# Kernel tuning notes

Hardware: AMD Instinct MI355X
Metric: run time of the kernel (lower is better)

Reference implementation:

```python
import jax, jax.numpy as jnp
import numpy as np
import math

DIM = 384
HEADS = 6
HEAD_DIM = DIM // HEADS
MLP_HIDDEN = int(DIM * 2.0)


def layer_norm(x, g, b, eps=1e-5):
    mu = jnp.mean(x, axis=-1, keepdims=True)
    var = jnp.mean((x - mu) ** 2, axis=-1, keepdims=True)
    return (x - mu) * jax.lax.rsqrt(var + eps) * g + b


def setup_inputs() -> dict:
    key = jax.random.key(0)
    ks = jax.random.split(key, 12)
    B, N = 4, 2048
    s = 0.02
    return {
        "x": jax.random.normal(ks[0], (B, N, DIM), dtype=jnp.float32),
        "pos": jax.random.normal(ks[1], (B, N, 3), dtype=jnp.float32),
        "qkv_w": jax.random.normal(ks[2], (DIM, 3 * DIM), dtype=jnp.float32) * s,
        "qkv_b": jnp.zeros((3 * DIM,), jnp.float32),
        "proj_w": jax.random.normal(ks[3], (DIM, DIM), dtype=jnp.float32) * s,
        "proj_b": jnp.zeros((DIM,), jnp.float32),
        "mlp_w1": jax.random.normal(ks[4], (DIM, MLP_HIDDEN), dtype=jnp.float32) * s,
        "mlp_b1": jnp.zeros((MLP_HIDDEN,), jnp.float32),
        "mlp_w2": jax.random.normal(ks[5], (MLP_HIDDEN, DIM), dtype=jnp.float32) * s,
        "mlp_b2": jnp.zeros((DIM,), jnp.float32),
        "ln1_g": jnp.ones((DIM,), jnp.float32),
        "ln1_b": jnp.zeros((DIM,), jnp.float32),
        "ln2_g": jnp.ones((DIM,), jnp.float32),
        "ln2_b": jnp.zeros((DIM,), jnp.float32),
    }


def reference(x, pos, qkv_w, qkv_b, proj_w, proj_b, mlp_w1, mlp_b1,
              mlp_w2, mlp_b2, ln1_g, ln1_b, ln2_g, ln2_b):
    B, N, D = x.shape
    H, Hd = HEADS, HEAD_DIM
    # qkv projection
    qkv = layer_norm(x, ln1_g, ln1_b) @ qkv_w + qkv_b          # [B,N,3D]
    qkv = qkv.reshape(B, N, 3, H, Hd)
    q = jnp.transpose(qkv[:, :, 0], (0, 2, 1, 3))               # [B,H,N,Hd]
    k = jnp.transpose(qkv[:, :, 1], (0, 2, 1, 3))
    v = jnp.transpose(qkv[:, :, 2], (0, 2, 1, 3))
    # pairwise squared-distance bias: exp(-||p_i - p_j||^2)
    rel = pos[:, :, None, :] - pos[:, None, :, :]               # [B,N,N,3]
    dist = jnp.exp(-jnp.sum(rel ** 2, axis=-1))                 # [B,N,N]
    scale = 1.0 / math.sqrt(Hd)
    attn = jnp.einsum('bhqd,bhkd->bhqk', q, k) * scale + dist[:, None, :, :]
    attn = jax.nn.softmax(attn, axis=-1)
    out = jnp.einsum('bhqk,bhkd->bhqd', attn, v)                # [B,H,N,Hd]
    out = jnp.transpose(out, (0, 2, 1, 3)).reshape(B, N, D)
    out = out @ proj_w + proj_b
    x = x + out
    h = layer_norm(x, ln2_g, ln2_b)
    h = jax.nn.gelu(h @ mlp_w1 + mlp_b1, approximate=False) @ mlp_w2 + mlp_b2
    return x + h
```

## Files before the change

kernel.cpp:

```cpp
#include <hip/hip_runtime.h>
#include <hip/hip_bf16.h>
#include <math.h>

#define DIMD 384
#define NHEADS 6
#define HD 64
#define MLPH 768
#define SEQ 2048
#define NBATCH 4
#define NTOK (NBATCH*SEQ)

typedef __hip_bfloat16 bf16;

typedef __attribute__((ext_vector_type(8))) short bf16x8;
typedef __attribute__((ext_vector_type(4))) float f32x4;

#define LOG2E 1.44269504088896340736f
#define SC2F 0.18033688011112042f

static __device__ inline float fexp2(float x) { return __builtin_amdgcn_exp2f(x); }

static __device__ inline f32x4 mfma16(bf16x8 a, bf16x8 b, f32x4 c) {
    return __builtin_amdgcn_mfma_f32_16x16x32_bf16(a, b, c, 0, 0, 0);
}

static __device__ inline unsigned int cvtpk(float lo, float hi) {
    unsigned int r;
    asm("v_cvt_pk_bf16_f32 %0, %1, %2" : "=v"(r) : "v"(lo), "v"(hi));
    return r;
}
static __device__ inline float bflo(unsigned int u) { return __builtin_bit_cast(float, u << 16); }
static __device__ inline float bfhi(unsigned int u) { return __builtin_bit_cast(float, u & 0xffff0000u); }

static __device__ inline void gld16(const void* g, void* l) {
    __builtin_amdgcn_global_load_lds(
        (const __attribute__((address_space(1))) unsigned int*)g,
        (__attribute__((address_space(3))) unsigned int*)l, 16, 0, 0);
}

static __device__ inline int xcd_swz(int wg, int nwg) {
    return (wg & 7) * (nwg >> 3) + (wg >> 3);
}

__global__ __launch_bounds__(256) void ln_k(const float* __restrict__ x,
                                            const float* __restrict__ gm,
                                            const float* __restrict__ bt,
                                            bf16* __restrict__ out) {
    int row = blockIdx.x * 4 + (threadIdx.x >> 6);
    int l = threadIdx.x & 63;
    const float* xr = x + (size_t)row * DIMD;
    float v[6];
#pragma unroll
    for (int j = 0; j < 6; ++j) v[j] = xr[l + 64 * j];
    float s = 0.f, s2 = 0.f;
#pragma unroll
    for (int j = 0; j < 6; ++j) { s += v[j]; s2 += v[j] * v[j]; }
#pragma unroll
    for (int m = 1; m < 64; m <<= 1) { s += __shfl_xor(s, m); s2 += __shfl_xor(s2, m); }
    float mu = s * (1.f / DIMD);
    float var = s2 * (1.f / DIMD) - mu * mu;
    float rs = rsqrtf(var + 1e-5f);
    bf16* orow = out + (size_t)row * DIMD;
#pragma unroll
    for (int j = 0; j < 6; ++j) {
        int i = l + 64 * j;
        orow[i] = __float2bfloat16((v[j] - mu) * rs * gm[i] + bt[i]);
    }
}

__global__ __launch_bounds__(256) void prep_k(const float* __restrict__ w1,
                                              const float* __restrict__ w2,
                                              const float* __restrict__ w3,
                                              const float* __restrict__ w4,
                                              bf16* __restrict__ o1,
                                              bf16* __restrict__ o2,
                                              bf16* __restrict__ o3,
                                              bf16* __restrict__ o4,
                                              const float* __restrict__ pos,
                                              bf16* __restrict__ DP,
                                              const float* __restrict__ x,
                                              const float* __restrict__ g1,
                                              const float* __restrict__ b1,
                                              bf16* __restrict__ xn) {
    __shared__ float shbuf[6144];
    int id = blockIdx.x;
    if (id < 1152) {
        float (*t)[33] = (float(*)[33])shbuf;
        const float* W; bf16* O; int K, N;
        if (id < 432)      { W = w1; O = o1; K = 384; N = 1152; }
        else if (id < 576) { W = w2; O = o2; K = 384; N = 384;  id -= 432; }
        else if (id < 864) { W = w3; O = o3; K = 384; N = 768;  id -= 576; }
        else               { W = w4; O = o4; K = 768; N = 384;  id -= 864; }
        int nbx = N >> 5;
        int nb = (id % nbx) * 32, kb = (id / nbx) * 32;
        int tx = threadIdx.x & 31, ty = threadIdx.x >> 5;
#pragma unroll
        for (int i = 0; i < 4; ++i)
            t[ty + 8 * i][tx] = W[(size_t)(kb + ty + 8 * i) * N + nb + tx];
        __syncthreads();
#pragma unroll
        for (int i = 0; i < 4; ++i)
            O[(size_t)(nb + ty + 8 * i) * K + kb + tx] = __float2bfloat16(t[tx][ty + 8 * i]);
    } else if (id < 1664) {
        int blk = id - 1152;
        int w = blk & 3, qt = (blk >> 2) & 31, b = blk >> 7;
        int l = threadIdx.x & 63, tt = threadIdx.x >> 6;
        int lq = l & 15, g = l >> 4;
        const float* posb = pos + (size_t)b * SEQ * 3;
        for (int i = threadIdx.x; i < 1536; i += 256)
            ((f32x4*)shbuf)[i] = ((const f32x4*)posb)[i];
        __syncthreads();
        int q = qt * 64 + w * 16 + lq;
        float px = shbuf[3 * q], py = shbuf[3 * q + 1], pz = shbuf[3 * q + 2];
        char* base = (char*)DP + (size_t)blk * 65536;
        for (int j = 0; j < 8; ++j) {
            int tt8 = tt * 8 + j;
#pragma unroll
            for (int m = 0; m < 2; ++m) {
                int k0 = tt8 * 64 + 32 * m + 4 * g;
                float a[24];
                *(f32x4*)&a[0]  = *(const f32x4*)&shbuf[3 * k0];
                *(f32x4*)&a[4]  = *(const f32x4*)&shbuf[3 * k0 + 4];
                *(f32x4*)&a[8]  = *(const f32x4*)&shbuf[3 * k0 + 8];
                *(f32x4*)&a[12] = *(const f32x4*)&shbuf[3 * (k0 + 16)];
                *(f32x4*)&a[16] = *(const f32x4*)&shbuf[3 * (k0 + 16) + 4];
                *(f32x4*)&a[20] = *(const f32x4*)&shbuf[3 * (k0 + 16) + 8];
                float o8[8];
#pragma unroll
                for (int r = 0; r < 8; ++r) {
                    float dx = px - a[3 * r], dy = py - a[3 * r + 1], dz = pz - a[3 * r + 2];
                    o8[r] = fexp2(-LOG2E * (dx * dx + dy * dy + dz * dz)) * LOG2E;
                }
                uint4 o;
                o.x = cvtpk(o8[0], o8[1]); o.y = cvtpk(o8[2], o8[3]);
                o.z = cvtpk(o8[4], o8[5]); o.w = cvtpk(o8[6], o8[7]);
                *(uint4*)(base + ((size_t)tt8 * 2 + m) * 1024 + l * 16) = o;
            }
        }
    } else {
        int row = (id - 1664) * 4 + (threadIdx.x >> 6);
        int l = threadIdx.x & 63;
        const float* xr = x + (size_t)row * DIMD;
        float v[6];
#pragma unroll
        for (int j = 0; j < 6; ++j) v[j] = xr[l + 64 * j];
        float s = 0.f, s2 = 0.f;
#pragma unroll
        for (int j = 0; j < 6; ++j) { s += v[j]; s2 += v[j] * v[j]; }
#pragma unroll
        for (int m = 1; m < 64; m <<= 1) { s += __shfl_xor(s, m); s2 += __shfl_xor(s2, m); }
        float mu = s * (1.f / DIMD);
        float var = s2 * (1.f / DIMD) - mu * mu;
        float rs = rsqrtf(var + 1e-5f);
        bf16* orow = xn + (size_t)row * DIMD;
#pragma unroll
        for (int j = 0; j < 6; ++j) {
            int i = l + 64 * j;
            orow[i] = __float2bfloat16((v[j] - mu) * rs * g1[i] + b1[i]);
        }
    }
}

template <int EPI, int NX, int KCN>
__global__ __launch_bounds__(256) void gemm128_k(const bf16* __restrict__ A,
                                                 const bf16* __restrict__ WT,
                                                 const float* __restrict__ bias,
                                                 bf16* __restrict__ ob0,
                                                 bf16* __restrict__ ob1,
                                                 bf16* __restrict__ ob2,
                                                 int K, int Nw) {
    __shared__ __align__(16) char Als[3][8192];
    __shared__ __align__(16) char Bls[3][8192];
    int tid = threadIdx.x;
    int w = tid >> 6, l = tid & 63;
    int c = l & 15, g = l >> 4;
    int wr = w >> 1, wc = w & 1;
    int swz = xcd_swz(blockIdx.x, gridDim.x);
    int m0 = (swz / NX) * 128, n0 = (swz % NX) * 128;
    const char* Ag = (const char*)A + (size_t)m0 * K * 2;
    const char* Bg = (const char*)WT + (size_t)n0 * K * 2;
    int K2 = K * 2;

    f32x4 acc[4][4];
#pragma unroll
    for (int mi = 0; mi < 4; ++mi)
#pragma unroll
        for (int ni = 0; ni < 4; ++ni) acc[mi][ni] = (f32x4){0.f, 0.f, 0.f, 0.f};

    auto stage = [&](int t, int bi) {
#pragma unroll
        for (int p = 0; p < 2; ++p) {
            int chunk = p * 256 + tid;
            int r = chunk >> 2;
            int cc = ((chunk & 3) ^ (r & 3)) << 4;
            gld16(Ag + (size_t)r * K2 + t * 64 + cc, &Als[bi][chunk * 16]);
            gld16(Bg + (size_t)r * K2 + t * 64 + cc, &Bls[bi][chunk * 16]);
        }
    };

    stage(0, 0);
    stage(1, 1);
#pragma unroll
    for (int t = 0; t < KCN; ++t) {
        asm volatile("s_waitcnt vmcnt(4)" ::: "memory");
        __builtin_amdgcn_sched_barrier(0);
        __builtin_amdgcn_s_barrier();
        __builtin_amdgcn_sched_barrier(0);

        int B0 = t % 3;
        bf16x8 af[4], bfr[4];
#pragma unroll
        for (int mi = 0; mi < 4; ++mi) {
            int row = wr * 64 + mi * 16 + c;
            __builtin_memcpy(&af[mi], &Als[B0][row * 64 + ((g ^ (row & 3)) << 4)], 16);
        }
#pragma unroll
        for (int ni = 0; ni < 4; ++ni) {
            int row = wc * 64 + ni * 16 + c;
            __builtin_memcpy(&bfr[ni], &Bls[B0][row * 64 + ((g ^ (row & 3)) << 4)], 16);
        }
        __builtin_amdgcn_s_setprio(1);
#pragma unroll
        for (int mi = 0; mi < 4; ++mi)
#pragma unroll
            for (int ni = 0; ni < 4; ++ni)
                acc[mi][ni] = mfma16(af[mi], bfr[ni], acc[mi][ni]);
        __builtin_amdgcn_s_setprio(0);

        __builtin_amdgcn_sched_barrier(0);
        int tn2 = t + 2 < KCN ? t + 2 : KCN - 1;
        stage(tn2, (t + 2) % 3);
        __builtin_amdgcn_sched_barrier(0);
    }

#pragma unroll
    for (int mi = 0; mi < 4; ++mi) {
#pragma unroll
        for (int ni = 0; ni < 4; ++ni) {
            int ntb = n0 + wc * 64 + ni * 16;
#pragma unroll
            for (int r = 0; r < 4; ++r) {
                int m = m0 + wr * 64 + mi * 16 + 4 * g + r;
                int n = ntb + c;
                float val = acc[mi][ni][r] + bias[n];
                if (EPI == 0) {
                    int which = ntb / DIMD;
                    int rem = ntb - which * DIMD;
                    int h = rem >> 6;
                    int d = (rem & 63) + c;
                    int b = m >> 11, s = m & (SEQ - 1);
                    if (which == 2) {
                        int slot = (s & ~31) + 8 * ((m & 15) >> 2) + 4 * ((m >> 4) & 1) + (m & 3);
                        ob2[(((size_t)b * NHEADS + h) * HD + d) * SEQ + slot] = __float2bfloat16(val);
                    } else {
                        if (which == 0) val *= SC2F;
                        bf16* dp = which == 0 ? ob0 : ob1;
                        dp[(((size_t)b * NHEADS + h) * SEQ + s) * HD + d] = __float2bfloat16(val);
                    }
                } else {
                    float ge = 0.5f * val * (1.0f + erff(val * 0.70710678118654752f));
                    ob0[(size_t)m * Nw + n] = __float2bfloat16(ge);
                }
            }
        }
    }
}

template <int NX, int KCN>
__global__ __launch_bounds__(256) void gemm_k(const bf16* __restrict__ A,
                                              const bf16* __restrict__ WT,
                                              const float* __restrict__ bias,
                                              const float* __restrict__ resid,
                                              float* __restrict__ outf,
                                              int K, int Nw) {
    __shared__ __align__(16) char Als[3][8192];
    __shared__ __align__(16) char Bls[3][8192];
    int tid = threadIdx.x;
    int w = tid >> 6, l = tid & 63;
    int c = l & 15, g = l >> 4;
    int swz = xcd_swz(blockIdx.x, gridDim.x);
    int m0 = (swz / NX) * 64, n0 = (swz % NX) * 64;
    const char* Ag = (const char*)A + (size_t)m0 * K * 2;
    const char* Bg = (const char*)WT + (size_t)n0 * K * 2;
    int K2 = K * 2;

    f32x4 acc[4];
#pragma unroll
    for (int nt = 0; nt < 4; ++nt) acc[nt] = (f32x4){0.f, 0.f, 0.f, 0.f};

    auto stage = [&](int t, int bi) {
#pragma unroll
        for (int p = 0; p < 2; ++p) {
            int chunk = p * 256 + tid;
            int r = chunk >> 3;
            int cc = ((chunk & 7) ^ (r & 7)) << 4;
            gld16(Ag + (size_t)r * K2 + t * 128 + cc, &Als[bi][chunk * 16]);
            gld16(Bg + (size_t)r * K2 + t * 128 + cc, &Bls[bi][chunk * 16]);
        }
    };

    stage(0, 0);
    stage(1, 1);
    int arow = (16 * w + c) * 128;
    int sw = c & 7;
#pragma unroll
    for (int t = 0; t < KCN; ++t) {
        asm volatile("s_waitcnt vmcnt(4)" ::: "memory");
        __builtin_amdgcn_sched_barrier(0);
        __builtin_amdgcn_s_barrier();
        __builtin_amdgcn_sched_barrier(0);

        int B0 = t % 3;
#pragma unroll
        for (int kk = 0; kk < 2; ++kk) {
            int ch = ((kk * 4 + g) ^ sw) << 4;
            bf16x8 af;
            __builtin_memcpy(&af, &Als[B0][arow + ch], 16);
            bf16x8 bfr[4];
#pragma unroll
            for (int nt = 0; nt < 4; ++nt)
                __builtin_memcpy(&bfr[nt], &Bls[B0][(nt * 16 + c) * 128 + ch], 16);
            __builtin_amdgcn_s_setprio(1);
#pragma unroll
            for (int nt = 0; nt < 4; ++nt)
                acc[nt] = mfma16(af, bfr[nt], acc[nt]);
            __builtin_amdgcn_s_setprio(0);
        }

        __builtin_amdgcn_sched_barrier(0);
        int tn2 = t + 2 < KCN ? t + 2 : KCN - 1;
        stage(tn2, (t + 2) % 3);
        __builtin_amdgcn_sched_barrier(0);
    }

#pragma unroll
    for (int nt = 0; nt < 4; ++nt) {
        int ntb = n0 + nt * 16;
#pragma unroll
        for (int r = 0; r < 4; ++r) {
            int m = m0 + 16 * w + 4 * g + r;
            int n = ntb + c;
            float val = acc[nt][r] + bias[n];
            val += resid[(size_t)m * Nw + n];
            outf[(size_t)m * Nw + n] = val;
        }
    }
}

__global__ __launch_bounds__(256) void attn_k(const bf16* __restrict__ q,
                                              const bf16* __restrict__ k,
                                              const bf16* __restrict__ vT,
                                              const bf16* __restrict__ DP,
                                              bf16* __restrict__ out) {
    __shared__ __align__(16) char Kls[3][4096];
    __shared__ __align__(16) char Vls[3][4096];

    int tid = threadIdx.x;
    int w = tid >> 6, l = tid & 63;
    int lq = l & 15, g = l >> 4;
    int swzb = xcd_swz(blockIdx.x, gridDim.x);
    int qt = swzb & 31;
    int bh = swzb >> 5;
    int b = bh / NHEADS, h = bh % NHEADS;
    int qrow = qt * 64 + w * 16 + lq;

    const bf16* qp = q + ((size_t)bh * SEQ + qrow) * HD + 8 * g;
    bf16x8 qf0 = *(const bf16x8*)qp;
    bf16x8 qf1 = *(const bf16x8*)(qp + 32);

    const char* kgb = (const char*)(k + (size_t)bh * SEQ * HD);
    const char* vgb = (const char*)(vT + (size_t)bh * HD * SEQ);
    const char* dpb = (const char*)DP + ((size_t)((b * 32 + qt) * 4 + w)) * 65536 + l * 16;

    f32x4 oacc[4];
#pragma unroll
    for (int dt = 0; dt < 4; ++dt) oacc[dt] = (f32x4){0.f, 0.f, 0.f, 0.f};
    f32x4 osum = (f32x4){0.f, 0.f, 0.f, 0.f};
    bf16x8 ones = {(short)0x3F80, (short)0x3F80, (short)0x3F80, (short)0x3F80,
                   (short)0x3F80, (short)0x3F80, (short)0x3F80, (short)0x3F80};

    int swq = lq & 7;
    int offA = lq * 128 + ((g ^ swq) << 4);
    int offB = lq * 128 + (((4 + g) ^ swq) << 4);
    int offV = lq * 64 + ((g ^ (lq & 3)) << 4);

    auto stage = [&](int t, int B2) {
        {
            int r = tid >> 3, c = tid & 7;
            int cc = (c ^ (r & 7)) << 4;
            gld16(kgb + (size_t)t * 4096 + r * 128 + cc, &Kls[B2][tid * 16]);
        }
        {
            int r = tid >> 2, c = tid & 3;
            int cc = (c ^ (r & 3)) << 4;
            gld16(vgb + (size_t)r * 4096 + t * 64 + cc, &Vls[B2][tid * 16]);
        }
    };

    stage(0, 0);
    uint4 cdp = *(const uint4*)(dpb);
    stage(1, 1);

    auto body = [&](int t, int B0, int B2) {
        asm volatile("s_waitcnt vmcnt(2)" ::: "memory");
        __builtin_amdgcn_sched_barrier(0);
        __builtin_amdgcn_s_barrier();
        __builtin_amdgcn_sched_barrier(0);

        const char* Kb = &Kls[B0][0];
        const char* Vb = &Vls[B0][0];
        f32x4 bc[2];
        bc[0] = (f32x4){bflo(cdp.x), bfhi(cdp.x), bflo(cdp.y), bfhi(cdp.y)};
        bc[1] = (f32x4){bflo(cdp.z), bfhi(cdp.z), bflo(cdp.w), bfhi(cdp.w)};
        f32x4 st[2];
        __builtin_amdgcn_s_setprio(1);
#pragma unroll
        for (int s = 0; s < 2; ++s) {
            bf16x8 klo, khi;
            __builtin_memcpy(&klo, Kb + s * 2048 + offA, 16);
            __builtin_memcpy(&khi, Kb + s * 2048 + offB, 16);
            st[s] = mfma16(klo, qf0, bc[s]);
            st[s] = mfma16(khi, qf1, st[s]);
        }
        __builtin_amdgcn_s_setprio(0);

        float p[8];
        p[0] = fexp2(st[0][0]);
        p[1] = fexp2(st[0][1]);
        p[2] = fexp2(st[0][2]);
        p[3] = fexp2(st[0][3]);
        p[4] = fexp2(st[1][0]);
        p[5] = fexp2(st[1][1]);
        p[6] = fexp2(st[1][2]);
        p[7] = fexp2(st[1][3]);

        unsigned int pw[4];
        pw[0] = cvtpk(p[0], p[1]);
        pw[1] = cvtpk(p[2], p[3]);
        pw[2] = cvtpk(p[4], p[5]);
        pw[3] = cvtpk(p[6], p[7]);
        bf16x8 pf;
        __builtin_memcpy(&pf, pw, 16);

        __builtin_amdgcn_s_setprio(1);
        osum = mfma16(ones, pf, osum);
#pragma unroll
        for (int dt = 0; dt < 4; ++dt) {
            bf16x8 vf;
            __builtin_memcpy(&vf, Vb + dt * 1024 + offV, 16);
            oacc[dt] = mfma16(vf, pf, oacc[dt]);
        }
        __builtin_amdgcn_s_setprio(0);

        __builtin_amdgcn_sched_barrier(0);
        int tn1 = t + 1 < 64 ? t + 1 : 63;
        uint4 nd = *(const uint4*)(dpb + (size_t)tn1 * 1024);
        __builtin_amdgcn_sched_barrier(0);
        int tn2 = t + 2 < 64 ? t + 2 : 63;
        stage(tn2, B2);
        __builtin_amdgcn_sched_barrier(0);
        cdp = nd;
    };

    for (int t = 0; t < 63; t += 3) {
        body(t + 0, 0, 2);
        body(t + 1, 1, 0);
        body(t + 2, 2, 1);
    }
    body(63, 0, 2);

    float inv = 1.f / osum[0];
    bf16* op = out + ((size_t)b * SEQ + qrow) * DIMD + h * HD + 4 * g;
#pragma unroll
    for (int dt = 0; dt < 4; ++dt) {
        unsigned int t2[2];
        t2[0] = cvtpk(oacc[dt][0] * inv, oacc[dt][1] * inv);
        t2[1] = cvtpk(oacc[dt][2] * inv, oacc[dt][3] * inv);
        __builtin_memcpy(op + dt * 16, t2, 8);
    }
}

extern "C" void kernel_launch(void* const* d_in, const int* in_sizes, int n_in,
                              void* d_out, int out_size, void* d_ws, size_t ws_size,
                              hipStream_t stream) {
    const float* x      = (const float*)d_in[0];
    const float* pos    = (const float*)d_in[1];
    const float* qkv_w  = (const float*)d_in[2];
    const float* qkv_b  = (const float*)d_in[3];
    const float* proj_w = (const float*)d_in[4];
    const float* proj_b = (const float*)d_in[5];
    const float* mlp_w1 = (const float*)d_in[6];
    const float* mlp_b1 = (const float*)d_in[7];
    const float* mlp_w2 = (const float*)d_in[8];
    const float* mlp_b2 = (const float*)d_in[9];
    const float* ln1_g  = (const float*)d_in[10];
    const float* ln1_b  = (const float*)d_in[11];
    const float* ln2_g  = (const float*)d_in[12];
    const float* ln2_b  = (const float*)d_in[13];

    char* p = (char*)d_ws;
    size_t off = 0;
    auto alloc = [&](size_t bytes) {
        char* r = p + off;
        off = (off + bytes + 255) & ~(size_t)255;
        return r;
    };
    bf16* WT1 = (bf16*)alloc((size_t)1152 * 384 * 2);
    bf16* WT2 = (bf16*)alloc((size_t)384 * 384 * 2);
    bf16* WT3 = (bf16*)alloc((size_t)384 * 768 * 2);
    bf16* WT4 = (bf16*)alloc((size_t)768 * 384 * 2);
    bf16* xn  = (bf16*)alloc((size_t)NTOK * DIMD * 2);
    bf16* xn2 = (bf16*)alloc((size_t)NTOK * DIMD * 2);
    bf16* qb  = (bf16*)alloc((size_t)NTOK * DIMD * 2);
    bf16* kb  = (bf16*)alloc((size_t)NTOK * DIMD * 2);
    bf16* vTb = (bf16*)alloc((size_t)NTOK * DIMD * 2);
    bf16* ao  = (bf16*)alloc((size_t)NTOK * DIMD * 2);
    float* x1 = (float*)alloc((size_t)NTOK * DIMD * 4);
    bf16* hh  = (bf16*)alloc((size_t)NTOK * MLPH * 2);
    bf16* dtab = (bf16*)alloc((size_t)NBATCH * SEQ * SEQ * 2);
    if (off > ws_size) return;

    prep_k<<<1152 + 512 + 2048, 256, 0, stream>>>(
        qkv_w, proj_w, mlp_w1, mlp_w2, WT1, WT2, WT3, WT4,
        pos, dtab, x, ln1_g, ln1_b, xn);

    gemm128_k<0, 9, 12><<<576, 256, 0, stream>>>(
        xn, WT1, qkv_b, qb, kb, vTb, 384, 1152);
    attn_k<<<NBATCH * NHEADS * (SEQ / 64), 256, 0, stream>>>(qb, kb, vTb, dtab, ao);
    gemm_k<6, 6><<<768, 256, 0, stream>>>(
        ao, WT2, proj_b, x, x1, 384, 384);
    ln_k<<<NTOK / 4, 256, 0, stream>>>(x1, ln2_g, ln2_b, xn2);
    gemm128_k<2, 6, 12><<<384, 256, 0, stream>>>(
        xn2, WT3, mlp_b1, hh, nullptr, nullptr, 384, 768);
    gemm_k<6, 12><<<768, 256, 0, stream>>>(
        hh, WT4, mlp_b2, x1, (float*)d_out, 768, 384);
}
```

Before: 130.4 us.

## Split attention KV range in two with partial outputs and a reduce kernel

```diff
diff --git a/kernel.cpp b/kernel.cpp
--- a/kernel.cpp
+++ b/kernel.cpp
@@ -351,7 +351,8 @@
                                               const bf16* __restrict__ k,
                                               const bf16* __restrict__ vT,
                                               const bf16* __restrict__ DP,
-                                              bf16* __restrict__ out) {
+                                              bf16* __restrict__ opart,
+                                              float* __restrict__ lsum) {
     __shared__ __align__(16) char Kls[3][4096];
     __shared__ __align__(16) char Vls[3][4096];
 
@@ -360,7 +361,9 @@
     int lq = l & 15, g = l >> 4;
     int swzb = xcd_swz(blockIdx.x, gridDim.x);
     int qt = swzb & 31;
-    int bh = swzb >> 5;
+    int bhh = swzb >> 5;
+    int half = bhh & 1;
+    int bh = bhh >> 1;
     int b = bh / NHEADS, h = bh % NHEADS;
     int qrow = qt * 64 + w * 16 + lq;
 
@@ -368,9 +371,10 @@
     bf16x8 qf0 = *(const bf16x8*)qp;
     bf16x8 qf1 = *(const bf16x8*)(qp + 32);
 
-    const char* kgb = (const char*)(k + (size_t)bh * SEQ * HD);
-    const char* vgb = (const char*)(vT + (size_t)bh * HD * SEQ);
-    const char* dpb = (const char*)DP + ((size_t)((b * 32 + qt) * 4 + w)) * 65536 + l * 16;
+    const char* kgb = (const char*)(k + (size_t)bh * SEQ * HD) + (size_t)half * 131072;
+    const char* vgb = (const char*)(vT + (size_t)bh * HD * SEQ) + (size_t)half * 2048;
+    const char* dpb = (const char*)DP + ((size_t)((b * 32 + qt) * 4 + w)) * 65536
+                      + (size_t)half * 32768 + l * 16;
 
     f32x4 oacc[4];
 #pragma unroll
@@ -382,7 +386,7 @@
     int swq = lq & 7;
     int offA = lq * 128 + ((g ^ swq) << 4);
     int offB = lq * 128 + (((4 + g) ^ swq) << 4);
-    int offV = lq * 64 + ((g ^ (lq & 3)) << 4);
+    int offV = lq * 64 + (((g ^ (lq & 3) ^ ((lq >> 2) & 3)) & 3) << 4);
 
     auto stage = [&](int t, int B2) {
         {
@@ -392,7 +396,7 @@
         }
         {
             int r = tid >> 2, c = tid & 3;
-            int cc = (c ^ (r & 3)) << 4;
+            int cc = ((c ^ (r & 3) ^ ((r >> 2) & 3)) & 3) << 4;
             gld16(vgb + (size_t)r * 4096 + t * 64 + cc, &Vls[B2][tid * 16]);
         }
     };
@@ -453,31 +457,58 @@
         __builtin_amdgcn_s_setprio(0);
 
         __builtin_amdgcn_sched_barrier(0);
-        int tn1 = t + 1 < 64 ? t + 1 : 63;
+        int tn1 = t + 1 < 32 ? t + 1 : 31;
         uint4 nd = *(const uint4*)(dpb + (size_t)tn1 * 1024);
         __builtin_amdgcn_sched_barrier(0);
-        int tn2 = t + 2 < 64 ? t + 2 : 63;
+        int tn2 = t + 2 < 32 ? t + 2 : 31;
         stage(tn2, B2);
         __builtin_amdgcn_sched_barrier(0);
         cdp = nd;
     };
 
-    for (int t = 0; t < 63; t += 3) {
+    for (int t = 0; t < 30; t += 3) {
         body(t + 0, 0, 2);
         body(t + 1, 1, 0);
         body(t + 2, 2, 1);
     }
-    body(63, 0, 2);
-
-    float inv = 1.f / osum[0];
-    bf16* op = out + ((size_t)b * SEQ + qrow) * DIMD + h * HD + 4 * g;
+    body(30, 0, 2);
+    body(31, 1, 0);
+
+    bf16* op = opart + (size_t)half * NTOK * DIMD
+               + ((size_t)b * SEQ + qrow) * DIMD + h * HD + 4 * g;
 #pragma unroll
     for (int dt = 0; dt < 4; ++dt) {
         unsigned int t2[2];
-        t2[0] = cvtpk(oacc[dt][0] * inv, oacc[dt][1] * inv);
-        t2[1] = cvtpk(oacc[dt][2] * inv, oacc[dt][3] * inv);
+        t2[0] = cvtpk(oacc[dt][0], oacc[dt][1]);
+        t2[1] = cvtpk(oacc[dt][2], oacc[dt][3]);
         __builtin_memcpy(op + dt * 16, t2, 8);
     }
+    if (g == 0) lsum[(size_t)bhh * SEQ + qrow] = osum[0];
+}
+
+__global__ __launch_bounds__(256) void reduce_k(const bf16* __restrict__ opart,
+                                                const float* __restrict__ lsum,
+                                                bf16* __restrict__ ao) {
+    size_t f = ((size_t)blockIdx.x * 256 + threadIdx.x) * 8;
+    int sg = (int)(f / DIMD);
+    int rem = (int)(f - (size_t)sg * DIMD);
+    int h = rem >> 6;
+    int b = sg >> 11;
+    int s = sg & (SEQ - 1);
+    int bh2 = (b * NHEADS + h) * 2;
+    float l0 = lsum[(size_t)bh2 * SEQ + s];
+    float l1 = lsum[(size_t)(bh2 + 1) * SEQ + s];
+    float inv = 1.f / (l0 + l1);
+    const unsigned int* p0 = (const unsigned int*)(opart + f);
+    const unsigned int* p1 = (const unsigned int*)(opart + (size_t)NTOK * DIMD + f);
+    uint4 u0 = *(const uint4*)p0;
+    uint4 u1 = *(const uint4*)p1;
+    unsigned int o[4];
+    o[0] = cvtpk((bflo(u0.x) + bflo(u1.x)) * inv, (bfhi(u0.x) + bfhi(u1.x)) * inv);
+    o[1] = cvtpk((bflo(u0.y) + bflo(u1.y)) * inv, (bfhi(u0.y) + bfhi(u1.y)) * inv);
+    o[2] = cvtpk((bflo(u0.z) + bflo(u1.z)) * inv, (bfhi(u0.z) + bfhi(u1.z)) * inv);
+    o[3] = cvtpk((bflo(u0.w) + bflo(u1.w)) * inv, (bfhi(u0.w) + bfhi(u1.w)) * inv);
+    *(uint4*)(ao + f) = *(uint4*)o;
 }
 
 extern "C" void kernel_launch(void* const* d_in, const int* in_sizes, int n_in,
@@ -518,6 +549,7 @@
     float* x1 = (float*)alloc((size_t)NTOK * DIMD * 4);
     bf16* hh  = (bf16*)alloc((size_t)NTOK * MLPH * 2);
     bf16* dtab = (bf16*)alloc((size_t)NBATCH * SEQ * SEQ * 2);
+    float* lsum = (float*)alloc((size_t)2 * NBATCH * NHEADS * SEQ * 4);
     if (off > ws_size) return;
 
     prep_k<<<1152 + 512 + 2048, 256, 0, stream>>>(
@@ -526,7 +558,8 @@
 
     gemm128_k<0, 9, 12><<<576, 256, 0, stream>>>(
         xn, WT1, qkv_b, qb, kb, vTb, 384, 1152);
-    attn_k<<<NBATCH * NHEADS * (SEQ / 64), 256, 0, stream>>>(qb, kb, vTb, dtab, ao);
+    attn_k<<<NBATCH * NHEADS * 2 * 32, 256, 0, stream>>>(qb, kb, vTb, dtab, hh, lsum);
+    reduce_k<<<NTOK * DIMD / 2048, 256, 0, stream>>>(hh, lsum, ao);
     gemm_k<6, 6><<<768, 256, 0, stream>>>(
         ao, WT2, proj_b, x, x1, 384, 384);
     ln_k<<<NTOK / 4, 256, 0, stream>>>(x1, ln2_g, ln2_b, xn2);
```

Measured after the change: 141.4 us. 8.5% more time.
